# Optimization experiments

Hardware: AMD Instinct MI355X
Metric: run time of the kernel (lower is better)

Reference implementation:

```python
import jax, jax.numpy as jnp
import numpy as np


def setup_inputs() -> dict:
    key = jax.random.key(0)
    kK, kQ = jax.random.split(key)
    B, S, D = 8, 2048, 512
    K = jax.random.normal(kK, (B, S, D), dtype=jnp.float32)
    Q = jax.random.normal(kQ, (B, S, D), dtype=jnp.float32)
    return {"K": K, "Q": Q}


def reference(K, Q):
    # K: [B, S_k, D], Q: [B, S_q, D]
    S_q = Q.shape[1]
    S_k = K.shape[1]
    # Causal mask: -inf strictly above the diagonal (k=1), as in np.triu(..., k=1)
    mask = jnp.where(jnp.triu(jnp.ones((S_q, S_k), dtype=bool), k=1), -jnp.inf, 0.0).astype(jnp.float32)
    # NOTE: original scales by sqrt(window_size_keys) (seq len), and adds mask BEFORE scaling.
    logits = (jnp.einsum('bqd,bkd->bqk', Q, K) + mask) / jnp.sqrt(jnp.float32(S_k))
    return jax.nn.softmax(logits, axis=-1)
```

## Files before the change

kernel.cpp:

```cpp
#include <hip/hip_runtime.h>
#include <hip/hip_bf16.h>
#include <math.h>

#define B_SZ 8
#define SEQ 2048
#define DIM 512

typedef __attribute__((ext_vector_type(8))) short bf16x8;
typedef __attribute__((ext_vector_type(8))) unsigned short u16x8;
typedef __attribute__((ext_vector_type(4))) float f32x4;

#define GLOBAL_AS __attribute__((address_space(1)))
#define LDS_AS __attribute__((address_space(3)))

__device__ __forceinline__ unsigned short f2bf(float f) {
    unsigned int u = __builtin_bit_cast(unsigned int, f);
    u += 0x7fffu + ((u >> 16) & 1u);
    return (unsigned short)(u >> 16);
}

__device__ __forceinline__ void load_lds16(const void* g, void* l) {
    __builtin_amdgcn_global_load_lds((const GLOBAL_AS unsigned int*)g,
                                     (LDS_AS unsigned int*)l, 16, 0, 0);
}

__global__ __launch_bounds__(256)
void convert_kernel(const float* __restrict__ Q, const float* __restrict__ K,
                    unsigned short* __restrict__ Qb, unsigned short* __restrict__ Kb,
                    float* __restrict__ sums) {
    const int half = (int)(((size_t)B_SZ * SEQ * DIM) / 8 / 256);
    const int bid = blockIdx.x;
    const int gi = bid * 256 + threadIdx.x;
    if (gi < B_SZ * SEQ) sums[gi] = 0.f;

    const float* src;
    unsigned short* dst;
    int i;
    if (bid < half) { src = Q; dst = Qb; i = gi; }
    else            { src = K; dst = Kb; i = gi - half * 256; }

    const float4* s = (const float4*)src;
    float4 a = s[2 * i];
    float4 b = s[2 * i + 1];
    u16x8 o;
    o[0] = f2bf(a.x); o[1] = f2bf(a.y); o[2] = f2bf(a.z); o[3] = f2bf(a.w);
    o[4] = f2bf(b.x); o[5] = f2bf(b.y); o[6] = f2bf(b.z); o[7] = f2bf(b.w);
    ((u16x8*)dst)[i] = o;
}

#define BM 128
#define BK 32
__global__ __launch_bounds__(256)
void logits_exp_mfma(const unsigned short* __restrict__ Qb, const unsigned short* __restrict__ Kb,
                     float* __restrict__ out, float* __restrict__ sums) {
    const int b = blockIdx.x, tk = blockIdx.y, tq = blockIdx.z;
    float* outb = out + (size_t)b * SEQ * SEQ;
    const int t = threadIdx.x;

    if (tk > tq) {
        const int r0 = t >> 5;
        const int c4 = t & 31;
        const float4 z = {0.f, 0.f, 0.f, 0.f};
        float* base = outb + (size_t)(tq * BM) * SEQ + tk * BM;
#pragma unroll
        for (int it = 0; it < 16; ++it)
            *(float4*)(base + (size_t)(it * 8 + r0) * SEQ + c4 * 4) = z;
        return;
    }

    __shared__ __align__(16) unsigned short a_lds[BM * BK];
    __shared__ __align__(16) unsigned short b_lds[BM * BK];

    const int wave = t >> 6;
    const int lane = t & 63;
    const int l16 = lane & 15;
    const int quad = lane >> 4;
    const int wm = wave >> 1;
    const int wn = wave & 1;

    const unsigned short* Qrow = Qb + ((size_t)b * SEQ + (size_t)tq * BM) * DIM;
    const unsigned short* Krow = Kb + ((size_t)b * SEQ + (size_t)tk * BM) * DIM;

    const int sr = lane >> 2;
    const int kg = lane & 3;

    f32x4 acc[4][4];
#pragma unroll
    for (int i = 0; i < 4; i++)
#pragma unroll
        for (int j = 0; j < 4; j++) acc[i][j] = (f32x4){0.f, 0.f, 0.f, 0.f};

    for (int k0 = 0; k0 < DIM; k0 += BK) {
#pragma unroll
        for (int j = wave; j < 8; j += 4) {
            int row = j * 16 + sr;
            load_lds16(Qrow + (size_t)row * DIM + k0 + kg * 8, &a_lds[(j * 16) * BK]);
            load_lds16(Krow + (size_t)row * DIM + k0 + kg * 8, &b_lds[(j * 16) * BK]);
        }
        __syncthreads();

        bf16x8 af[4], bfr[4];
#pragma unroll
        for (int mi = 0; mi < 4; mi++)
            af[mi] = *(const bf16x8*)&a_lds[(wm * 64 + mi * 16 + l16) * BK + quad * 8];
#pragma unroll
        for (int ni = 0; ni < 4; ni++)
            bfr[ni] = *(const bf16x8*)&b_lds[(wn * 64 + ni * 16 + l16) * BK + quad * 8];
#pragma unroll
        for (int mi = 0; mi < 4; mi++)
#pragma unroll
            for (int ni = 0; ni < 4; ni++)
                acc[mi][ni] = __builtin_amdgcn_mfma_f32_16x16x32_bf16(af[mi], bfr[ni], acc[mi][ni], 0, 0, 0);
        __syncthreads();
    }

    const float scale = 0.02209708691207961f;
    const bool diag = (tk == tq);
    float* sums_b = sums + (size_t)b * SEQ;

#pragma unroll
    for (int mi = 0; mi < 4; mi++) {
#pragma unroll
        for (int r = 0; r < 4; r++) {
            const int row_l = wm * 64 + mi * 16 + quad * 4 + r;
            const int row = tq * BM + row_l;
            float rsum = 0.f;
#pragma unroll
            for (int ni = 0; ni < 4; ni++) {
                const int col = tk * BM + wn * 64 + ni * 16 + l16;
                float e;
                if (diag && col > row) e = 0.f;
                else e = __expf(acc[mi][ni][r] * scale);
                outb[(size_t)row * SEQ + col] = e;
                rsum += e;
            }
            rsum += __shfl_xor(rsum, 1);
            rsum += __shfl_xor(rsum, 2);
            rsum += __shfl_xor(rsum, 4);
            rsum += __shfl_xor(rsum, 8);
            if (l16 == 0) atomicAdd(&sums_b[row], rsum);
        }
    }
}

__global__ __launch_bounds__(256)
void scale_kernel(float* __restrict__ out, const float* __restrict__ sums) {
    const int q = blockIdx.x & (SEQ - 1);
    const int b = blockIdx.x >> 11;
    float* row = out + ((size_t)b * SEQ + q) * SEQ;
    const float inv = 1.0f / sums[blockIdx.x];
    const int n = q + 1;
    const int t = threadIdx.x;
#pragma unroll
    for (int j = 0; j < 2; ++j) {
        int k0 = (t + j * 256) * 4;
        if (k0 < n) {
            float4 x = *(const float4*)(row + k0);
            x.x *= inv; x.y *= inv; x.z *= inv; x.w *= inv;
            *(float4*)(row + k0) = x;
        }
    }
}

#define TS 64
#define DC 128
#define LSTRIDE (DC + 8)
__global__ __launch_bounds__(256)
void logits_fallback(const float* __restrict__ Q, const float* __restrict__ K,
                     float* __restrict__ out) {
    const int tk = blockIdx.x, tq = blockIdx.y, b = blockIdx.z;
    if (tk > tq) return;
    __shared__ __align__(16) unsigned short qs[TS * LSTRIDE];
    __shared__ __align__(16) unsigned short ks[TS * LSTRIDE];
    const int t = threadIdx.x;
    const int wave = t >> 6, lane = t & 63, l16 = lane & 15, quad = lane >> 4;
    const float* Qb = Q + ((size_t)b * SEQ + (size_t)tq * TS) * DIM;
    const float* Kb = K + ((size_t)b * SEQ + (size_t)tk * TS) * DIM;
    f32x4 acc[4];
#pragma unroll
    for (int i = 0; i < 4; i++) acc[i] = (f32x4){0.f, 0.f, 0.f, 0.f};
    for (int c = 0; c < DIM; c += DC) {
        __syncthreads();
#pragma unroll
        for (int i = 0; i < 8; i++) {
            int idx = t + i * 256;
            int row = idx >> 5, c4 = idx & 31;
            float4 qv = *(const float4*)(Qb + row * DIM + c + c4 * 4);
            float4 kv = *(const float4*)(Kb + row * DIM + c + c4 * 4);
            ushort4 qh = { f2bf(qv.x), f2bf(qv.y), f2bf(qv.z), f2bf(qv.w) };
            ushort4 kh = { f2bf(kv.x), f2bf(kv.y), f2bf(kv.z), f2bf(kv.w) };
            *(ushort4*)&qs[row * LSTRIDE + c4 * 4] = qh;
            *(ushort4*)&ks[row * LSTRIDE + c4 * 4] = kh;
        }
        __syncthreads();
#pragma unroll
        for (int d = 0; d < DC; d += 32) {
            bf16x8 afrag = *(const bf16x8*)&qs[(wave * 16 + l16) * LSTRIDE + d + quad * 8];
#pragma unroll
            for (int nt = 0; nt < 4; nt++) {
                bf16x8 bfrag = *(const bf16x8*)&ks[(nt * 16 + l16) * LSTRIDE + d + quad * 8];
                acc[nt] = __builtin_amdgcn_mfma_f32_16x16x32_bf16(afrag, bfrag, acc[nt], 0, 0, 0);
            }
        }
    }
    const float scale = 0.02209708691207961f;
    float* outb = out + (size_t)b * SEQ * SEQ;
#pragma unroll
    for (int nt = 0; nt < 4; nt++) {
        int col = tk * TS + nt * 16 + l16;
#pragma unroll
        for (int r = 0; r < 4; r++) {
            int row = tq * TS + wave * 16 + quad * 4 + r;
            outb[(size_t)row * SEQ + col] = acc[nt][r] * scale;
        }
    }
}

__global__ __launch_bounds__(256)
void softmax_kernel(float* __restrict__ out) {
    const int q = blockIdx.x & (SEQ - 1);
    const int b = blockIdx.x >> 11;
    float* row = out + ((size_t)b * SEQ + q) * SEQ;
    const int t = threadIdx.x;
    const int lane = t & 63;
    const int wave = t >> 6;
    const int n = q + 1;

    __shared__ float red[8];

    float4 v[2];
    float m = -INFINITY;
#pragma unroll
    for (int j = 0; j < 2; j++) {
        int k0 = (t + j * 256) * 4;
        if (k0 < n) {
            float4 x = *(const float4*)(row + k0);
            x.y = (k0 + 1 < n) ? x.y : -INFINITY;
            x.z = (k0 + 2 < n) ? x.z : -INFINITY;
            x.w = (k0 + 3 < n) ? x.w : -INFINITY;
            v[j] = x;
            m = fmaxf(m, fmaxf(fmaxf(x.x, x.y), fmaxf(x.z, x.w)));
        } else {
            v[j] = (float4){-INFINITY, -INFINITY, -INFINITY, -INFINITY};
        }
    }
#pragma unroll
    for (int off = 1; off < 64; off <<= 1) m = fmaxf(m, __shfl_xor(m, off));
    if (lane == 0) red[wave] = m;
    __syncthreads();
    m = fmaxf(fmaxf(red[0], red[1]), fmaxf(red[2], red[3]));

    float s = 0.f;
#pragma unroll
    for (int j = 0; j < 2; j++) {
        float4 e;
        e.x = __expf(v[j].x - m);
        e.y = __expf(v[j].y - m);
        e.z = __expf(v[j].z - m);
        e.w = __expf(v[j].w - m);
        v[j] = e;
        s += e.x + e.y + e.z + e.w;
    }
#pragma unroll
    for (int off = 1; off < 64; off <<= 1) s += __shfl_xor(s, off);
    if (lane == 0) red[4 + wave] = s;
    __syncthreads();
    s = red[4] + red[5] + red[6] + red[7];
    const float inv = 1.0f / s;

#pragma unroll
    for (int j = 0; j < 2; j++) {
        int k0 = (t + j * 256) * 4;
        float4 e = v[j];
        e.x *= inv; e.y *= inv; e.z *= inv; e.w *= inv;
        *(float4*)(row + k0) = e;
    }
}

extern "C" void kernel_launch(void* const* d_in, const int* in_sizes, int n_in,
                              void* d_out, int out_size, void* d_ws, size_t ws_size,
                              hipStream_t stream) {
    const float* Kp = (const float*)d_in[0];
    const float* Qp = (const float*)d_in[1];
    float* out = (float*)d_out;

    const size_t nElem = (size_t)B_SZ * SEQ * DIM;
    const size_t bfBytes = nElem * sizeof(unsigned short);
    const size_t sumsBytes = (size_t)B_SZ * SEQ * sizeof(float);

    if (ws_size >= 2 * bfBytes + sumsBytes) {
        unsigned short* Qbf = (unsigned short*)d_ws;
        unsigned short* Kbf = Qbf + nElem;
        float* sums = (float*)((char*)d_ws + 2 * bfBytes);
        const int half = (int)(nElem / 8 / 256);
        convert_kernel<<<dim3(2 * half), dim3(256), 0, stream>>>(Qp, Kp, Qbf, Kbf, sums);
        logits_exp_mfma<<<dim3(B_SZ, SEQ / BM, SEQ / BM), dim3(256), 0, stream>>>(Qbf, Kbf, out, sums);
        scale_kernel<<<dim3(B_SZ * SEQ), dim3(256), 0, stream>>>(out, sums);
    } else {
        logits_fallback<<<dim3(SEQ / TS, SEQ / TS, B_SZ), dim3(256), 0, stream>>>(Qp, Kp, out);
        softmax_kernel<<<dim3(B_SZ * SEQ), dim3(256), 0, stream>>>(out);
    }
}
```

Baseline: 227.5 us.

## Use 256x256 tiles with 4-slot LDS pipeline and swizzled staging

Expands the logits GEMM tile from 128x128 to 256x256 with 512 threads (8 waves), each wave computing a 128x64 sub-tile. Global-to-LDS loads now go through a 4-slot ring, staged two k-steps ahead and waited on with explicit vmcnt, and the LDS layout is XOR-swizzled to avoid bank conflicts. MFMA phases are raised with s_setprio and interleaved with the prefetch issues. The goal is to hide load latency and raise arithmetic intensity. In exchange, the coarser tiles waste more work on the causal diagonal, the grid is smaller (fewer blocks), and register pressure is higher (128 accumulators).

```diff
diff --git a/kernel.cpp b/kernel.cpp
--- a/kernel.cpp
+++ b/kernel.cpp
@@ -48,9 +48,14 @@
     ((u16x8*)dst)[i] = o;
 }
 
-#define BM 128
-#define BK 32
-__global__ __launch_bounds__(256)
+#define STAGE_CHUNK(gbase, slot, tens, j, kcol)                               \
+    { const int srow_ = (j) * 128 + wv * 16 + (lane >> 2);                    \
+      const int scc_ = lane & 3;                                              \
+      load_lds16((gbase) + (size_t)srow_ * DIM + (kcol) +                     \
+                     ((scc_ ^ (srow_ & 3)) << 3),                             \
+                 &lds[slot][tens][(j) * 4096 + wv * 512]); }
+
+__global__ __launch_bounds__(512, 2)
 void logits_exp_mfma(const unsigned short* __restrict__ Qb, const unsigned short* __restrict__ Kb,
                      float* __restrict__ out, float* __restrict__ sums) {
     const int b = blockIdx.x, tk = blockIdx.y, tq = blockIdx.z;
@@ -58,60 +63,86 @@
     const int t = threadIdx.x;
 
     if (tk > tq) {
-        const int r0 = t >> 5;
-        const int c4 = t & 31;
+        const int r0 = t >> 6;
+        const int c4 = t & 63;
         const float4 z = {0.f, 0.f, 0.f, 0.f};
-        float* base = outb + (size_t)(tq * BM) * SEQ + tk * BM;
-#pragma unroll
-        for (int it = 0; it < 16; ++it)
+        float* base = outb + (size_t)(tq * 256) * SEQ + tk * 256;
+#pragma unroll
+        for (int it = 0; it < 32; ++it)
             *(float4*)(base + (size_t)(it * 8 + r0) * SEQ + c4 * 4) = z;
         return;
     }
 
-    __shared__ __align__(16) unsigned short a_lds[BM * BK];
-    __shared__ __align__(16) unsigned short b_lds[BM * BK];
-
-    const int wave = t >> 6;
+    __shared__ __align__(16) unsigned short lds[4][2][8192];
+
+    const int wv = t >> 6;
     const int lane = t & 63;
     const int l16 = lane & 15;
     const int quad = lane >> 4;
-    const int wm = wave >> 1;
-    const int wn = wave & 1;
-
-    const unsigned short* Qrow = Qb + ((size_t)b * SEQ + (size_t)tq * BM) * DIM;
-    const unsigned short* Krow = Kb + ((size_t)b * SEQ + (size_t)tk * BM) * DIM;
-
-    const int sr = lane >> 2;
-    const int kg = lane & 3;
-
-    f32x4 acc[4][4];
-#pragma unroll
-    for (int i = 0; i < 4; i++)
+    const int wm = wv >> 2;
+    const int wn = wv & 3;
+
+    const unsigned short* Qt = Qb + ((size_t)b * SEQ + (size_t)tq * 256) * DIM;
+    const unsigned short* Kt = Kb + ((size_t)b * SEQ + (size_t)tk * 256) * DIM;
+
+    f32x4 acc[8][4];
+#pragma unroll
+    for (int i = 0; i < 8; i++)
 #pragma unroll
         for (int j = 0; j < 4; j++) acc[i][j] = (f32x4){0.f, 0.f, 0.f, 0.f};
 
-    for (int k0 = 0; k0 < DIM; k0 += BK) {
-#pragma unroll
-        for (int j = wave; j < 8; j += 4) {
-            int row = j * 16 + sr;
-            load_lds16(Qrow + (size_t)row * DIM + k0 + kg * 8, &a_lds[(j * 16) * BK]);
-            load_lds16(Krow + (size_t)row * DIM + k0 + kg * 8, &b_lds[(j * 16) * BK]);
-        }
-        __syncthreads();
-
-        bf16x8 af[4], bfr[4];
-#pragma unroll
-        for (int mi = 0; mi < 4; mi++)
-            af[mi] = *(const bf16x8*)&a_lds[(wm * 64 + mi * 16 + l16) * BK + quad * 8];
-#pragma unroll
-        for (int ni = 0; ni < 4; ni++)
-            bfr[ni] = *(const bf16x8*)&b_lds[(wn * 64 + ni * 16 + l16) * BK + quad * 8];
-#pragma unroll
-        for (int mi = 0; mi < 4; mi++)
-#pragma unroll
-            for (int ni = 0; ni < 4; ni++)
-                acc[mi][ni] = __builtin_amdgcn_mfma_f32_16x16x32_bf16(af[mi], bfr[ni], acc[mi][ni], 0, 0, 0);
-        __syncthreads();
+    STAGE_CHUNK(Qt, 0, 0, 0, 0);  STAGE_CHUNK(Qt, 0, 0, 1, 0);
+    STAGE_CHUNK(Kt, 0, 1, 0, 0);  STAGE_CHUNK(Kt, 0, 1, 1, 0);
+    STAGE_CHUNK(Qt, 1, 0, 0, 32); STAGE_CHUNK(Qt, 1, 0, 1, 32);
+    STAGE_CHUNK(Kt, 1, 1, 0, 32); STAGE_CHUNK(Kt, 1, 1, 1, 32);
+
+    for (int k = 0; k < 16; ++k) {
+        const int slot = k & 3;
+        const int nslot = (k + 2) & 3;
+        const int kc2 = (k + 2) * 32;
+
+        if (k < 15) asm volatile("s_waitcnt vmcnt(4)" ::: "memory");
+        else        asm volatile("s_waitcnt vmcnt(0)" ::: "memory");
+        __builtin_amdgcn_s_barrier();
+
+        bf16x8 a0[4], bq[4];
+#pragma unroll
+        for (int m = 0; m < 4; ++m) {
+            const int row = wm * 128 + m * 16 + l16;
+            a0[m] = *(const bf16x8*)&lds[slot][0][row * 32 + ((quad ^ (row & 3)) << 3)];
+        }
+#pragma unroll
+        for (int n = 0; n < 4; ++n) {
+            const int row = wn * 64 + n * 16 + l16;
+            bq[n] = *(const bf16x8*)&lds[slot][1][row * 32 + ((quad ^ (row & 3)) << 3)];
+        }
+        if (k < 14) { STAGE_CHUNK(Qt, nslot, 0, 0, kc2); STAGE_CHUNK(Qt, nslot, 0, 1, kc2); }
+        __builtin_amdgcn_s_barrier();
+        __builtin_amdgcn_s_setprio(1);
+#pragma unroll
+        for (int m = 0; m < 4; ++m)
+#pragma unroll
+            for (int n = 0; n < 4; ++n)
+                acc[m][n] = __builtin_amdgcn_mfma_f32_16x16x32_bf16(a0[m], bq[n], acc[m][n], 0, 0, 0);
+        __builtin_amdgcn_s_setprio(0);
+        __builtin_amdgcn_s_barrier();
+
+        bf16x8 a1[4];
+#pragma unroll
+        for (int m = 0; m < 4; ++m) {
+            const int row = wm * 128 + 64 + m * 16 + l16;
+            a1[m] = *(const bf16x8*)&lds[slot][0][row * 32 + ((quad ^ (row & 3)) << 3)];
+        }
+        if (k < 14) { STAGE_CHUNK(Kt, nslot, 1, 0, kc2); STAGE_CHUNK(Kt, nslot, 1, 1, kc2); }
+        __builtin_amdgcn_s_barrier();
+        __builtin_amdgcn_s_setprio(1);
+#pragma unroll
+        for (int m = 0; m < 4; ++m)
+#pragma unroll
+            for (int n = 0; n < 4; ++n)
+                acc[4 + m][n] = __builtin_amdgcn_mfma_f32_16x16x32_bf16(a1[m], bq[n], acc[4 + m][n], 0, 0, 0);
+        __builtin_amdgcn_s_setprio(0);
+        __builtin_amdgcn_s_barrier();
     }
 
     const float scale = 0.02209708691207961f;
@@ -119,15 +150,14 @@
     float* sums_b = sums + (size_t)b * SEQ;
 
 #pragma unroll
-    for (int mi = 0; mi < 4; mi++) {
+    for (int mi = 0; mi < 8; mi++) {
 #pragma unroll
         for (int r = 0; r < 4; r++) {
-            const int row_l = wm * 64 + mi * 16 + quad * 4 + r;
-            const int row = tq * BM + row_l;
+            const int row = tq * 256 + wm * 128 + mi * 16 + quad * 4 + r;
             float rsum = 0.f;
 #pragma unroll
             for (int ni = 0; ni < 4; ni++) {
-                const int col = tk * BM + wn * 64 + ni * 16 + l16;
+                const int col = tk * 256 + wn * 64 + ni * 16 + l16;
                 float e;
                 if (diag && col > row) e = 0.f;
                 else e = __expf(acc[mi][ni][r] * scale);
@@ -294,7 +324,7 @@
         float* sums = (float*)((char*)d_ws + 2 * bfBytes);
         const int half = (int)(nElem / 8 / 256);
         convert_kernel<<<dim3(2 * half), dim3(256), 0, stream>>>(Qp, Kp, Qbf, Kbf, sums);
-        logits_exp_mfma<<<dim3(B_SZ, SEQ / BM, SEQ / BM), dim3(256), 0, stream>>>(Qbf, Kbf, out, sums);
+        logits_exp_mfma<<<dim3(B_SZ, SEQ / 256, SEQ / 256), dim3(512), 0, stream>>>(Qbf, Kbf, out, sums);
         scale_kernel<<<dim3(B_SZ * SEQ), dim3(256), 0, stream>>>(out, sums);
     } else {
         logits_fallback<<<dim3(SEQ / TS, SEQ / TS, B_SZ), dim3(256), 0, stream>>>(Qp, Kp, out);
```

Measured after the change: 237.4 us. 1.04x slower.
